# Kernel tuning notes

Measured on AMD Instinct MI355X. Metric: run time of the kernel, lower is better.

Reference implementation:

```python
import jax, jax.numpy as jnp
import numpy as np


def setup_inputs() -> dict:
    key = jax.random.key(0)
    k1, k2, k3, k4 = jax.random.split(key, 4)
    B, Cin, H, W = 16, 64, 96, 96
    D, O, KH, KW, S = 100, 256, 3, 3, 3
    x = jax.random.normal(k1, (B, Cin, H, W), dtype=jnp.float32)
    dictionary = jax.random.normal(k2, (D, Cin, KH, KW), dtype=jnp.float32) * 0.05
    lookup_coefficients = jax.random.normal(k3, (O, KH, KW, S), dtype=jnp.float32) * 0.1
    lookup_indices = jax.random.randint(k4, (O, KH, KW, S), 0, D, dtype=jnp.int64)
    return {
        "x": x,
        "dictionary": dictionary,
        "lookup_coefficients": lookup_coefficients,
        "lookup_indices": lookup_indices,
    }


def reference(x, dictionary, lookup_coefficients, lookup_indices):
    # Dense conv with the small dictionary: [B, Cin, H, W] x [D, Cin, kh, kw] -> [B, D, Oh, Ow]
    conv_out = jax.lax.conv_general_dilated(
        x, dictionary,
        window_strides=(1, 1),
        padding=((1, 1), (1, 1)),
        dimension_numbers=("NCHW", "OIHW", "NCHW"),
    )
    O = lookup_coefficients.shape[0]
    D = dictionary.shape[0]
    # Flatten kernel-position and sparsity axes: each (position, slot) contributes
    # coeff * conv_out[:, idx] to output channel o; COO duplicates sum.
    idx = lookup_indices.reshape(O, -1)      # [O, P*S]
    coeff = lookup_coefficients.reshape(O, -1)  # [O, P*S]
    # Scatter-add into a per-output-channel weight over dictionary entries: W[o, d]
    Wmat = jnp.zeros((O, D), dtype=conv_out.dtype).at[jnp.arange(O)[:, None], idx].add(coeff)
    # Gather-weighted-sum == sparse (O x D) matmul against conv_out channels
    out = jnp.einsum("od,bdhw->bohw", Wmat, conv_out)
    return out
```

## Files before the change

### kernel.cpp

```cpp
#include <hip/hip_runtime.h>

#define NB   16
#define CIN  64
#define HH   96
#define WW   96
#define DD   100
#define OO   256
#define NWG  (NB * HH)

typedef __attribute__((ext_vector_type(8))) short  bf16x8;
typedef __attribute__((ext_vector_type(4))) float  f32x4;

static __device__ __forceinline__ unsigned short f32_to_bf16(float f) {
    unsigned int u = __float_as_uint(f);
    u += 0x7FFFu + ((u >> 16) & 1u);
    return (unsigned short)(u >> 16);
}

__global__ __launch_bounds__(256) void prep_kernel(
    const float* __restrict__ x, const float* __restrict__ dict,
    const float* __restrict__ coeff, const int* __restrict__ idx,
    unsigned short* __restrict__ x2, unsigned short* __restrict__ weff2)
{
    __shared__ unsigned short lds[CIN * 100];
    __shared__ float wrow[DD];
    const int blk = blockIdx.x, tid = threadIdx.x;

    if (blk < NWG) {
        const int b = blk / HH, h = blk % HH;
        for (int it = 0; it < 6; ++it) {
            int i = tid + it * 256;
            int c = i / 24, w4 = i % 24;
            float4 v = *reinterpret_cast<const float4*>(
                x + (((size_t)(b * CIN + c) * HH + h) * WW + w4 * 4));
            ushort4 u;
            u.x = f32_to_bf16(v.x); u.y = f32_to_bf16(v.y);
            u.z = f32_to_bf16(v.z); u.w = f32_to_bf16(v.w);
            *reinterpret_cast<ushort4*>(&lds[c * 100 + w4 * 4]) = u;
        }
        __syncthreads();
        for (int it = 0; it < 6; ++it) {
            int i = tid + it * 256;
            int w = i / 16, c = (i % 16) * 4;
            ushort4 u;
            u.x = lds[(c + 0) * 100 + w];
            u.y = lds[(c + 1) * 100 + w];
            u.z = lds[(c + 2) * 100 + w];
            u.w = lds[(c + 3) * 100 + w];
            *reinterpret_cast<ushort4*>(x2 + (((size_t)(b * HH + h) * WW + w) * CIN + c)) = u;
        }
    } else {
        const int o = blk - NWG;
        if (tid < DD) wrow[tid] = 0.f;
        __syncthreads();
        if (tid == 0) {
            for (int s = 0; s < 27; ++s) wrow[idx[o * 27 + s]] += coeff[o * 27 + s];
        }
        __syncthreads();
        for (int j = tid; j < 576; j += 256) {
            int kpos = j >> 6, c = j & 63;
            float s = 0.f;
            for (int d = 0; d < DD; ++d)
                s += wrow[d] * dict[d * 576 + c * 9 + kpos];
            int otile = o >> 4, ks = c >> 5;
            int lane8 = (o & 15) | (((c >> 3) & 3) << 4);
            weff2[((size_t)((kpos * 16 + otile) * 2 + ks)) * 512 + lane8 * 8 + (c & 7)]
                = f32_to_bf16(s);
        }
    }
}

__global__ __launch_bounds__(512, 4) void conv_kernel(
    const unsigned short* __restrict__ x2,
    const unsigned short* __restrict__ weff2,
    float* __restrict__ out)
{
    __shared__ unsigned short xs[3 * 98 * 64];

    const int wg  = blockIdx.x;
    const int swz = (wg & 7) * (NWG / 8) + (wg >> 3);
    const int b = swz / HH, h = swz % HH;
    const int tid = threadIdx.x;
    const int lane = tid & 63, wid = tid >> 6;
    const int wm = wid >> 2, wn = wid & 3;

    char* xsb = reinterpret_cast<char*>(xs);

    for (int it = 0; it < 5; ++it) {
        int chunk = tid + it * 512;
        if (chunk < 2304) {
            int r = chunk / 768, rem = chunk % 768;
            int w = rem >> 3, c0 = (rem & 7) * 8;
            int hp = h - 1 + r;
            int wp = w + 1;
            int lb = r * 12544 + (((wp * 64 + c0) * 2) ^ ((wp & 7) << 4));
            bf16x8 v = {0,0,0,0,0,0,0,0};
            if (hp >= 0 && hp < HH)
                v = *reinterpret_cast<const bf16x8*>(
                    x2 + (((size_t)(b * HH + hp) * WW + w) * CIN + c0));
            *reinterpret_cast<bf16x8*>(xsb + lb) = v;
        }
    }
    if (tid < 48) {
        int r = tid / 16, side = (tid & 15) >> 3, ci = tid & 7;
        int wp = side ? 97 : 0;
        int lb = r * 12544 + (((wp * 64 + ci * 8) * 2) ^ ((wp & 7) << 4));
        bf16x8 z = {0,0,0,0,0,0,0,0};
        *reinterpret_cast<bf16x8*>(xsb + lb) = z;
    }

    f32x4 acc[3][4];
#pragma unroll
    for (int m = 0; m < 3; ++m)
#pragma unroll
        for (int n = 0; n < 4; ++n)
            acc[m][n] = (f32x4){0.f, 0.f, 0.f, 0.f};

    __syncthreads();

    for (int kpos = 0; kpos < 9; ++kpos) {
        bf16x8 bfr[2][4];
#pragma unroll
        for (int ks = 0; ks < 2; ++ks)
#pragma unroll
            for (int n = 0; n < 4; ++n) {
                int frag = (kpos * 16 + (wn * 4 + n)) * 2 + ks;
                bfr[ks][n] = *reinterpret_cast<const bf16x8*>(
                    weff2 + (size_t)frag * 512 + lane * 8);
            }

        const int r = kpos / 3, dw = kpos % 3;
        const int xbase = r * 12544;
#pragma unroll
        for (int ks = 0; ks < 2; ++ks) {
            const int c = ks * 32 + (lane >> 4) * 8;
#pragma unroll
            for (int m = 0; m < 3; ++m) {
                int wp = wm * 48 + m * 16 + (lane & 15) + dw;
                int lb = xbase + (((wp * 64 + c) * 2) ^ ((wp & 7) << 4));
                bf16x8 a = *reinterpret_cast<const bf16x8*>(xsb + lb);
#pragma unroll
                for (int n = 0; n < 4; ++n)
                    acc[m][n] = __builtin_amdgcn_mfma_f32_16x16x32_bf16(
                        a, bfr[ks][n], acc[m][n], 0, 0, 0);
            }
        }
    }

#pragma unroll
    for (int m = 0; m < 3; ++m) {
#pragma unroll
        for (int n = 0; n < 4; ++n) {
            int o = wn * 64 + n * 16 + (lane & 15);
            int w = wm * 48 + m * 16 + (lane >> 4) * 4;
            *reinterpret_cast<float4*>(
                out + (((size_t)(b * OO + o) * HH + h) * WW + w))
                = *reinterpret_cast<float4*>(&acc[m][n]);
        }
    }
}

extern "C" void kernel_launch(void* const* d_in, const int* in_sizes, int n_in,
                              void* d_out, int out_size, void* d_ws, size_t ws_size,
                              hipStream_t stream) {
    const float* x     = (const float*)d_in[0];
    const float* dict  = (const float*)d_in[1];
    const float* coeff = (const float*)d_in[2];
    const int*   idx   = (const int*)d_in[3];
    float* out = (float*)d_out;

    char* ws = (char*)d_ws;
    unsigned short* weff2 = (unsigned short*)ws;
    unsigned short* x2    = (unsigned short*)(ws + 1048576);

    prep_kernel<<<NWG + OO, 256, 0, stream>>>(x, dict, coeff, idx, x2, weff2);
    conv_kernel<<<NWG, 512, 0, stream>>>(x2, weff2, out);
}
```

Before: 82.19 us.

## Fuse fp32-to-bf16 input transpose into conv kernel and double-buffer weight fragments

The separate x-to-bf16 NHWC prep pass is removed. The conv kernel now reads fp32 NCHW rows directly, converts them, and writes them transposed into LDS with a new swizzle. This drops the intermediate x2 write and re-read through global memory. Weight fragments are prefetched one step ahead in two register buffers across a fully unrolled 18-step loop. The cost is scalar 2-byte LDS stores, each block re-reading three fp32 rows, and higher register pressure.

```diff
diff --git a/kernel.cpp b/kernel.cpp
--- a/kernel.cpp
+++ b/kernel.cpp
@@ -17,61 +17,34 @@
     return (unsigned short)(u >> 16);
 }
 
-__global__ __launch_bounds__(256) void prep_kernel(
-    const float* __restrict__ x, const float* __restrict__ dict,
-    const float* __restrict__ coeff, const int* __restrict__ idx,
-    unsigned short* __restrict__ x2, unsigned short* __restrict__ weff2)
+#define FSWZ(wp) ((((wp) ^ ((wp) >> 3)) & 7) << 4)
+
+__global__ __launch_bounds__(256) void weff_prep(
+    const float* __restrict__ dict, const float* __restrict__ coeff,
+    const int* __restrict__ idx, unsigned short* __restrict__ weff2)
 {
-    __shared__ unsigned short lds[CIN * 100];
     __shared__ float wrow[DD];
-    const int blk = blockIdx.x, tid = threadIdx.x;
-
-    if (blk < NWG) {
-        const int b = blk / HH, h = blk % HH;
-        for (int it = 0; it < 6; ++it) {
-            int i = tid + it * 256;
-            int c = i / 24, w4 = i % 24;
-            float4 v = *reinterpret_cast<const float4*>(
-                x + (((size_t)(b * CIN + c) * HH + h) * WW + w4 * 4));
-            ushort4 u;
-            u.x = f32_to_bf16(v.x); u.y = f32_to_bf16(v.y);
-            u.z = f32_to_bf16(v.z); u.w = f32_to_bf16(v.w);
-            *reinterpret_cast<ushort4*>(&lds[c * 100 + w4 * 4]) = u;
-        }
-        __syncthreads();
-        for (int it = 0; it < 6; ++it) {
-            int i = tid + it * 256;
-            int w = i / 16, c = (i % 16) * 4;
-            ushort4 u;
-            u.x = lds[(c + 0) * 100 + w];
-            u.y = lds[(c + 1) * 100 + w];
-            u.z = lds[(c + 2) * 100 + w];
-            u.w = lds[(c + 3) * 100 + w];
-            *reinterpret_cast<ushort4*>(x2 + (((size_t)(b * HH + h) * WW + w) * CIN + c)) = u;
-        }
-    } else {
-        const int o = blk - NWG;
-        if (tid < DD) wrow[tid] = 0.f;
-        __syncthreads();
-        if (tid == 0) {
-            for (int s = 0; s < 27; ++s) wrow[idx[o * 27 + s]] += coeff[o * 27 + s];
-        }
-        __syncthreads();
-        for (int j = tid; j < 576; j += 256) {
-            int kpos = j >> 6, c = j & 63;
-            float s = 0.f;
-            for (int d = 0; d < DD; ++d)
-                s += wrow[d] * dict[d * 576 + c * 9 + kpos];
-            int otile = o >> 4, ks = c >> 5;
-            int lane8 = (o & 15) | (((c >> 3) & 3) << 4);
-            weff2[((size_t)((kpos * 16 + otile) * 2 + ks)) * 512 + lane8 * 8 + (c & 7)]
-                = f32_to_bf16(s);
-        }
+    const int o = blockIdx.x, tid = threadIdx.x;
+    if (tid < DD) wrow[tid] = 0.f;
+    __syncthreads();
+    if (tid == 0) {
+        for (int s = 0; s < 27; ++s) wrow[idx[o * 27 + s]] += coeff[o * 27 + s];
+    }
+    __syncthreads();
+    for (int j = tid; j < 576; j += 256) {
+        int kpos = j >> 6, c = j & 63;
+        float s = 0.f;
+        for (int d = 0; d < DD; ++d)
+            s += wrow[d] * dict[d * 576 + c * 9 + kpos];
+        int otile = o >> 4, ks = c >> 5;
+        int lane8 = (o & 15) | (((c >> 3) & 3) << 4);
+        weff2[((size_t)(kpos * 32 + otile * 2 + ks)) * 512 + lane8 * 8 + (c & 7)]
+            = f32_to_bf16(s);
     }
 }
 
 __global__ __launch_bounds__(512, 4) void conv_kernel(
-    const unsigned short* __restrict__ x2,
+    const float* __restrict__ x,
     const unsigned short* __restrict__ weff2,
     float* __restrict__ out)
 {
@@ -86,25 +59,38 @@
 
     char* xsb = reinterpret_cast<char*>(xs);
 
-    for (int it = 0; it < 5; ++it) {
-        int chunk = tid + it * 512;
-        if (chunk < 2304) {
-            int r = chunk / 768, rem = chunk % 768;
-            int w = rem >> 3, c0 = (rem & 7) * 8;
-            int hp = h - 1 + r;
-            int wp = w + 1;
-            int lb = r * 12544 + (((wp * 64 + c0) * 2) ^ ((wp & 7) << 4));
-            bf16x8 v = {0,0,0,0,0,0,0,0};
-            if (hp >= 0 && hp < HH)
-                v = *reinterpret_cast<const bf16x8*>(
-                    x2 + (((size_t)(b * HH + hp) * WW + w) * CIN + c0));
-            *reinterpret_cast<bf16x8*>(xsb + lb) = v;
+    const unsigned short* wp_base = weff2 + (size_t)(wn * 8) * 512 + lane * 8;
+    bf16x8 bA[4], bB[4];
+#pragma unroll
+    for (int n = 0; n < 4; ++n)
+        bA[n] = *reinterpret_cast<const bf16x8*>(wp_base + (n * 2 + 0) * 512);
+#pragma unroll
+    for (int n = 0; n < 4; ++n)
+        bB[n] = *reinterpret_cast<const bf16x8*>(wp_base + (n * 2 + 1) * 512);
+
+    const float* xb = x + (size_t)b * CIN * HH * WW;
+#pragma unroll
+    for (int it = 0; it < 9; ++it) {
+        int k = tid + it * 512;
+        int r = k / 1536, rem = k % 1536;
+        int c = rem / 24, w4 = rem % 24;
+        int hp = h - 1 + r;
+        float4 v = {0.f, 0.f, 0.f, 0.f};
+        if (hp >= 0 && hp < HH)
+            v = *reinterpret_cast<const float4*>(xb + ((size_t)c * HH + hp) * WW + w4 * 4);
+        int rb = r * 12544;
+#pragma unroll
+        for (int j = 0; j < 4; ++j) {
+            int wpos = w4 * 4 + j + 1;
+            float f = (j == 0) ? v.x : (j == 1) ? v.y : (j == 2) ? v.z : v.w;
+            int lb = rb + ((wpos * 128 + c * 2) ^ FSWZ(wpos));
+            *reinterpret_cast<unsigned short*>(xsb + lb) = f32_to_bf16(f);
         }
     }
     if (tid < 48) {
         int r = tid / 16, side = (tid & 15) >> 3, ci = tid & 7;
-        int wp = side ? 97 : 0;
-        int lb = r * 12544 + (((wp * 64 + ci * 8) * 2) ^ ((wp & 7) << 4));
+        int wpos = side ? 97 : 0;
+        int lb = r * 12544 + ((wpos * 128 + ci * 16) ^ FSWZ(wpos));
         bf16x8 z = {0,0,0,0,0,0,0,0};
         *reinterpret_cast<bf16x8*>(xsb + lb) = z;
     }
@@ -118,31 +104,31 @@
 
     __syncthreads();
 
-    for (int kpos = 0; kpos < 9; ++kpos) {
-        bf16x8 bfr[2][4];
+    const int wbase = wm * 48 + (lane & 15);
+
 #pragma unroll
-        for (int ks = 0; ks < 2; ++ks)
+    for (int s = 0; s < 18; ++s) {
+        const int kpos = s >> 1, ks = s & 1;
+        const int r = kpos / 3, dw = kpos % 3;
+        const int cb2 = (ks * 32 + (lane >> 4) * 8) * 2;
+        const int rb = r * 12544;
+#pragma unroll
+        for (int m = 0; m < 3; ++m) {
+            int wpos = wbase + m * 16 + dw;
+            int lb = rb + ((wpos * 128 + cb2) ^ FSWZ(wpos));
+            bf16x8 a = *reinterpret_cast<const bf16x8*>(xsb + lb);
+#pragma unroll
+            for (int n = 0; n < 4; ++n)
+                acc[m][n] = __builtin_amdgcn_mfma_f32_16x16x32_bf16(
+                    a, (s & 1) ? bB[n] : bA[n], acc[m][n], 0, 0, 0);
+        }
+        if (s < 16) {
+            const int s2 = s + 2;
+            const int off = ((s2 >> 1) * 32 + (s2 & 1)) * 512;
 #pragma unroll
             for (int n = 0; n < 4; ++n) {
-                int frag = (kpos * 16 + (wn * 4 + n)) * 2 + ks;
-                bfr[ks][n] = *reinterpret_cast<const bf16x8*>(
-                    weff2 + (size_t)frag * 512 + lane * 8);
-            }
-
-        const int r = kpos / 3, dw = kpos % 3;
-        const int xbase = r * 12544;
-#pragma unroll
-        for (int ks = 0; ks < 2; ++ks) {
-            const int c = ks * 32 + (lane >> 4) * 8;
-#pragma unroll
-            for (int m = 0; m < 3; ++m) {
-                int wp = wm * 48 + m * 16 + (lane & 15) + dw;
-                int lb = xbase + (((wp * 64 + c) * 2) ^ ((wp & 7) << 4));
-                bf16x8 a = *reinterpret_cast<const bf16x8*>(xsb + lb);
-#pragma unroll
-                for (int n = 0; n < 4; ++n)
-                    acc[m][n] = __builtin_amdgcn_mfma_f32_16x16x32_bf16(
-                        a, bfr[ks][n], acc[m][n], 0, 0, 0);
+                bf16x8 v = *reinterpret_cast<const bf16x8*>(wp_base + off + n * 2 * 512);
+                if ((s & 1) == 0) bA[n] = v; else bB[n] = v;
             }
         }
     }
@@ -169,10 +155,8 @@
     const int*   idx   = (const int*)d_in[3];
     float* out = (float*)d_out;
 
-    char* ws = (char*)d_ws;
-    unsigned short* weff2 = (unsigned short*)ws;
-    unsigned short* x2    = (unsigned short*)(ws + 1048576);
+    unsigned short* weff2 = (unsigned short*)d_ws;
 
-    prep_kernel<<<NWG + OO, 256, 0, stream>>>(x, dict, coeff, idx, x2, weff2);
-    conv_kernel<<<NWG, 512, 0, stream>>>(x2, weff2, out);
+    weff_prep<<<OO, 256, 0, stream>>>(dict, coeff, idx, weff2);
+    conv_kernel<<<NWG, 512, 0, stream>>>(x, weff2, out);
 }
```

After: 82.59 us. Within noise of the previous version (+0.5%).
